# Performance work log

Hardware: AMD Instinct MI355X
Metric: run time of the kernel (lower is better)

The kernel has to match this reference:

```python
import math
import jax, jax.numpy as jnp
import numpy as np

LN_EPS = 1e-5


def _layernorm(x, g, b):
    m = jnp.mean(x, axis=-1, keepdims=True)
    v = jnp.var(x, axis=-1, keepdims=True)
    return (x - m) / jnp.sqrt(v + LN_EPS) * g + b


def setup_inputs() -> dict:
    key = jax.random.key(0)
    ks = jax.random.split(key, 14)
    B, C, H, W = 8, 96, 224, 224
    dim, hidden = 96, int(96 * 4.0)

    def lin(k, i, o):
        return jax.random.normal(k, (i, o), jnp.float32) * 0.02

    return {
        "x": jax.random.normal(ks[0], (B, C, H, W), jnp.float32),
        "entropy_map": jax.random.uniform(ks[1], (B, 1, H, W), jnp.float32),
        "beta": jnp.float32(1.0),
        "wq": lin(ks[2], dim, dim), "bq": jnp.zeros((dim,), jnp.float32),
        "wk": lin(ks[3], dim, dim), "bk": jnp.zeros((dim,), jnp.float32),
        "wv": lin(ks[4], dim, dim), "bv": jnp.zeros((dim,), jnp.float32),
        "wo": lin(ks[5], dim, dim), "bo": jnp.zeros((dim,), jnp.float32),
        "ln1_g": jnp.ones((dim,), jnp.float32), "ln1_b": jnp.zeros((dim,), jnp.float32),
        "ln2_g": jnp.ones((dim,), jnp.float32), "ln2_b": jnp.zeros((dim,), jnp.float32),
        "w_fc1": lin(ks[6], dim, hidden), "b_fc1": jnp.zeros((hidden,), jnp.float32),
        "w_fc2": lin(ks[7], hidden, dim), "b_fc2": jnp.zeros((dim,), jnp.float32),
    }


def reference(x, entropy_map, beta, wq, bq, wk, bk, wv, bv, wo, bo,
              ln1_g, ln1_b, ln2_g, ln2_b, w_fc1, b_fc1, w_fc2, b_fc2):
    B, C, H, W = x.shape
    ws = 7
    num_heads = 4
    hd = C // num_heads
    nHw, nWw = H // ws, W // ws
    N = ws * ws

    # (B,C,H,W) -> (B,H,W,C), norm1
    xt = jnp.transpose(x, (0, 2, 3, 1))
    xn = _layernorm(xt, ln1_g, ln1_b)

    # window partition -> (B*nW, N, C)
    xw = xn.reshape(B, nHw, ws, nWw, ws, C).transpose(0, 1, 3, 2, 4, 5).reshape(-1, N, C)
    ew = entropy_map.transpose(0, 2, 3, 1).reshape(B, nHw, ws, nWw, ws, 1)
    ew = ew.transpose(0, 1, 3, 2, 4, 5).reshape(-1, N, 1)  # (Bw, N, 1)

    Bw = xw.shape[0]
    q = (jnp.einsum('bnc,cd->bnd', xw, wq) + bq).reshape(Bw, N, num_heads, hd).transpose(0, 2, 1, 3)
    k = (jnp.einsum('bnc,cd->bnd', xw, wk) + bk).reshape(Bw, N, num_heads, hd).transpose(0, 2, 1, 3)
    v = (jnp.einsum('bnc,cd->bnd', xw, wv) + bv).reshape(Bw, N, num_heads, hd).transpose(0, 2, 1, 3)

    scores = jnp.einsum('bhqd,bhkd->bhqk', q, k) / math.sqrt(hd)
    attn = jax.nn.softmax(scores, axis=-1)

    # entropy gating: per-query factor (Bw,1,N,1), then renormalize over keys
    gating = jnp.exp(-beta * ew)[:, None, :, :]
    attn = attn * gating
    attn = attn / (jnp.sum(attn, axis=-1, keepdims=True) + 1e-9)

    out = jnp.einsum('bhqk,bhkd->bhqd', attn, v).transpose(0, 2, 1, 3).reshape(Bw, N, C)
    out = jnp.einsum('bnc,cd->bnd', out, wo) + bo

    # window merge -> (B,H,W,C)
    out = out.reshape(B, nHw, nWw, ws, ws, C).transpose(0, 1, 3, 2, 4, 5).reshape(B, H, W, C)

    x_res = xt + out  # (B,H,W,C)

    # MLP branch
    xn2 = _layernorm(x_res, ln2_g, ln2_b)
    h = jax.nn.gelu(jnp.einsum('bhwc,cd->bhwd', xn2, w_fc1) + b_fc1, approximate=False)
    mlp_out = jnp.einsum('bhwd,dc->bhwc', h, w_fc2) + b_fc2

    x_out = x_res + mlp_out
    return jnp.transpose(x_out, (0, 3, 1, 2))  # (B,C,H,W)
```

## Files before the change

kernel.cpp:

```cpp
#include <hip/hip_runtime.h>
#include <hip/hip_bf16.h>
#include <math.h>

typedef __attribute__((ext_vector_type(8))) short short8;
typedef __attribute__((ext_vector_type(4))) float f32x4;
typedef __attribute__((ext_vector_type(4))) unsigned int uint4v;

struct __align__(8) U2 { unsigned int x, y; };

#define DEVI static __device__ __forceinline__

DEVI unsigned pk1(float f){ unsigned u = __float_as_uint(f); return (u + 0x7fffu + ((u>>16)&1u)) >> 16; }
DEVI unsigned pk2(float a, float b){
  __hip_bfloat162 h = __float22bfloat162_rn(float2{a, b});
  union { __hip_bfloat162 h; unsigned u; } c; c.h = h; return c.u;
}
DEVI float bfu(unsigned hs){ return __uint_as_float((hs & 0xffffu) << 16); }

DEVI short8 lds8(const unsigned short* p){
  union { short8 v; U2 u[2]; } f;
  f.u[0] = *(const U2*)p;
  f.u[1] = *(const U2*)(p + 4);
  return f.v;
}
DEVI short8 mk8(unsigned a, unsigned b, unsigned c, unsigned d){
  union { short8 v; unsigned u[4]; } f; f.u[0]=a; f.u[1]=b; f.u[2]=c; f.u[3]=d; return f.v;
}
DEVI short8 zero8(){ return mk8(0,0,0,0); }
DEVI short8 gfrag(const unsigned short* p){ union { short8 v; uint4v u; } f; f.u = *(const uint4v*)p; return f.v; }
DEVI f32x4 MFMA(short8 a, short8 b, f32x4 c){ return __builtin_amdgcn_mfma_f32_16x16x32_bf16(a, b, c, 0, 0, 0); }
DEVI void st2(unsigned short* p, unsigned lo, unsigned hi){ U2 t; t.x=lo; t.y=hi; *(U2*)p = t; }

DEVI float fastrcp(float x){ float r; asm("v_rcp_f32 %0, %1" : "=v"(r) : "v"(x)); return r; }
DEVI float gelu_f(float v){
  float z2 = fmaf(v*v*v, -0.07135481627f, -1.5957691216f*v);
  return v * fastrcp(1.f + __expf(z2));
}

__global__ __launch_bounds__(256) void prep_kernel(
    const float* __restrict__ wq, const float* __restrict__ wk,
    const float* __restrict__ wv, const float* __restrict__ wo,
    const float* __restrict__ w1, const float* __restrict__ w2,
    unsigned short* __restrict__ wfr)
{
  int i = blockIdx.x * 256 + threadIdx.x;
  if (i >= 110592) return;
  int j = i & 7, lane = (i >> 3) & 63, fr = i >> 9;
  int ln = lane & 15, lg = lane >> 4;
  float v;
  if (fr < 18)      { int s = fr;       int mt = s/3,  kb = s%3;  v = wq[(32*kb + 8*lg + j)*96  + 16*mt + ln] * 0.20412414523193150818f; }
  else if (fr < 36) { int s = fr - 18;  int mt = s/3,  kb = s%3;  v = wk[(32*kb + 8*lg + j)*96  + 16*mt + ln]; }
  else if (fr < 54) { int s = fr - 36;  int mt = s/3,  kb = s%3;  v = wv[(32*kb + 8*lg + j)*96  + 16*mt + ln]; }
  else if (fr < 72) { int s = fr - 54;  int mt = s/3,  kb = s%3;  v = wo[(32*kb + 8*lg + j)*96  + 16*mt + ln]; }
  else if (fr < 144){ int s = fr - 72;  int mt = s/3,  kb = s%3;  v = w1[(32*kb + 8*lg + j)*384 + 16*mt + ln]; }
  else              { int s = fr - 144; int mt = s/12, kb = s%12; v = w2[(32*kb + 8*lg + j)*96  + 16*mt + ln]; }
  wfr[i] = (unsigned short)pk1(v);
}

__global__ __launch_bounds__(256, 3) void attn_kernel(
    const float* __restrict__ x, const float* __restrict__ emap,
    const float* __restrict__ beta_p,
    const float* __restrict__ bq, const float* __restrict__ bk,
    const float* __restrict__ bv, const float* __restrict__ bo,
    const float* __restrict__ g1, const float* __restrict__ b1,
    const unsigned short* __restrict__ wfr,
    unsigned short* __restrict__ xres)
{
  __shared__ __align__(16) char smem[48448];
  unsigned short* XN = (unsigned short*)(smem);
  unsigned short* VT = (unsigned short*)(smem);
  unsigned short* QS = (unsigned short*)(smem + 14144);
  unsigned short* KS = (unsigned short*)(smem + 26944);
  unsigned short* PB = (unsigned short*)(smem + 39744);

  const int tid = threadIdx.x;
  const int lane = tid & 63;
  const int w = tid >> 6, lg = lane >> 4, ln = lane & 15;

  int bid = blockIdx.x;
  int bw  = ((bid & 7) << 10) | (bid >> 3);
  const int b  = bw >> 10;
  const int rr = bw & 1023;
  const int h0w = (rr >> 5) * 7;
  const int w0w = (rr & 31) * 7;

  const int t = 16*w + ln;

  float xv[24];
  float ewv = 0.f;
  {
    if (t < 49){
      size_t pixloc = (size_t)(h0w + t/7)*224 + w0w + t%7;
      const float* xp = x + (size_t)(b*96 + 4*lg)*50176 + pixloc;
#pragma unroll
      for (int mt = 0; mt < 6; ++mt)
#pragma unroll
        for (int r = 0; r < 4; ++r) xv[mt*4+r] = xp[(size_t)(16*mt + r)*50176];
      ewv = emap[(size_t)b*50176 + pixloc];
    } else {
#pragma unroll
      for (int i = 0; i < 24; ++i) xv[i] = 0.f;
    }
    float s = 0.f, s2 = 0.f;
#pragma unroll
    for (int i = 0; i < 24; ++i){ s += xv[i]; s2 += xv[i]*xv[i]; }
    s  += __shfl_xor(s, 16);  s  += __shfl_xor(s, 32);
    s2 += __shfl_xor(s2, 16); s2 += __shfl_xor(s2, 32);
    float m = s * (1.f/96.f);
    float var = s2 * (1.f/96.f) - m*m;
    float rstd = rsqrtf(var + 1e-5f);
    unsigned short* row = XN + t*100;
    if (t < 49){
#pragma unroll
      for (int mt = 0; mt < 6; ++mt){
        int c0 = 16*mt + 4*lg;
        st2(row + c0,
            pk2((xv[4*mt+0]-m)*rstd*g1[c0+0]+b1[c0+0], (xv[4*mt+1]-m)*rstd*g1[c0+1]+b1[c0+1]),
            pk2((xv[4*mt+2]-m)*rstd*g1[c0+2]+b1[c0+2], (xv[4*mt+3]-m)*rstd*g1[c0+3]+b1[c0+3]));
      }
    } else {
#pragma unroll
      for (int mt = 0; mt < 6; ++mt) st2(row + 16*mt + 4*lg, 0u, 0u);
    }
  }

  short8 bx0 = lds8(XN + t*100 + 0  + 8*lg);
  short8 bx1 = lds8(XN + t*100 + 32 + 8*lg);
  short8 bx2 = lds8(XN + t*100 + 64 + 8*lg);
  __syncthreads();

  {
#pragma unroll
    for (int mt = 0; mt < 6; ++mt){
      int d0 = 16*mt + 4*lg;
      f32x4 aq, ak;
#pragma unroll
      for (int r = 0; r < 4; ++r){ aq[r] = bq[d0+r]*0.20412414523193150818f; ak[r] = bk[d0+r]; }
      aq = MFMA(gfrag(wfr +        (mt*3+0)*512 + lane*8), bx0, aq);
      aq = MFMA(gfrag(wfr +        (mt*3+1)*512 + lane*8), bx1, aq);
      aq = MFMA(gfrag(wfr +        (mt*3+2)*512 + lane*8), bx2, aq);
      ak = MFMA(gfrag(wfr + 9216 + (mt*3+0)*512 + lane*8), bx0, ak);
      ak = MFMA(gfrag(wfr + 9216 + (mt*3+1)*512 + lane*8), bx1, ak);
      ak = MFMA(gfrag(wfr + 9216 + (mt*3+2)*512 + lane*8), bx2, ak);
      st2(QS + t*100 + d0, pk2(aq[0],aq[1]), pk2(aq[2],aq[3]));
      st2(KS + t*100 + d0, pk2(ak[0],ak[1]), pk2(ak[2],ak[3]));
    }
#pragma unroll
    for (int mt = 0; mt < 6; ++mt){
      int d0 = 16*mt + 4*lg;
      f32x4 av;
#pragma unroll
      for (int r = 0; r < 4; ++r) av[r] = bv[d0+r];
      av = MFMA(gfrag(wfr + 18432 + (mt*3+0)*512 + lane*8), bx0, av);
      av = MFMA(gfrag(wfr + 18432 + (mt*3+1)*512 + lane*8), bx1, av);
      av = MFMA(gfrag(wfr + 18432 + (mt*3+2)*512 + lane*8), bx2, av);
#pragma unroll
      for (int r = 0; r < 4; ++r) VT[(d0+r)*68 + t] = (unsigned short)pk1(av[r]);
    }
  }
  __syncthreads();

  const float beta = beta_p[0];
  const float gq   = __expf(-beta * ewv);
  const float gfac = gq / (gq + 1e-9f);

  f32x4 mz;  mz[0]=0.f; mz[1]=0.f; mz[2]=0.f; mz[3]=0.f;
  f32x4 m3;
#pragma unroll
  for (int r = 0; r < 4; ++r) m3[r] = (4*lg + r >= 1) ? -50.f : 0.f;

  unsigned short* PBw = PB + (w*16 + ln)*68;

#pragma unroll
  for (int hp = 0; hp < 2; ++hp){
    const int h0 = 2*hp, h1 = 2*hp + 1;

    short8 bqf0 = (lg < 3) ? lds8(QS + t*100 + 24*h0 + 8*lg) : zero8();
    short8 bqf1 = (lg < 3) ? lds8(QS + t*100 + 24*h1 + 8*lg) : zero8();
    f32x4 sv0[4], sv1[4];
#pragma unroll
    for (int mt = 0; mt < 4; ++mt){
      short8 af0 = (lg < 3) ? lds8(KS + (16*mt+ln)*100 + 24*h0 + 8*lg) : zero8();
      short8 af1 = (lg < 3) ? lds8(KS + (16*mt+ln)*100 + 24*h1 + 8*lg) : zero8();
      f32x4 ci = (mt == 3) ? m3 : mz;
      sv0[mt] = MFMA(af0, bqf0, ci);
      sv1[mt] = MFMA(af1, bqf1, ci);
    }

    float vv0[16], vv1[16];
    float ss0 = 0.f, ss1 = 0.f;
#pragma unroll
    for (int i = 0; i < 16; ++i){
      float e0 = __expf(sv0[i>>2][i&3]); vv0[i] = e0; ss0 += e0;
      float e1 = __expf(sv1[i>>2][i&3]); vv1[i] = e1; ss1 += e1;
    }
    ss0 += __shfl_xor(ss0, 16);  ss1 += __shfl_xor(ss1, 16);
    ss0 += __shfl_xor(ss0, 32);  ss1 += __shfl_xor(ss1, 32);
    float inv0 = gfac * fastrcp(ss0);
    float inv1 = gfac * fastrcp(ss1);

#pragma unroll
    for (int mt = 0; mt < 4; ++mt)
      st2(PBw + 16*mt + 4*lg,
          pk2(vv0[4*mt+0], vv0[4*mt+1]), pk2(vv0[4*mt+2], vv0[4*mt+3]));
    short8 pf00 = lds8(PBw + 0  + 8*lg);
    short8 pf01 = lds8(PBw + 32 + 8*lg);

#pragma unroll
    for (int mt = 0; mt < 4; ++mt)
      st2(PBw + 16*mt + 4*lg,
          pk2(vv1[4*mt+0], vv1[4*mt+1]), pk2(vv1[4*mt+2], vv1[4*mt+3]));
    short8 pf10 = lds8(PBw + 0  + 8*lg);
    short8 pf11 = lds8(PBw + 32 + 8*lg);

#pragma unroll
    for (int mt = 0; mt < 2; ++mt){
      f32x4 pv0; pv0[0]=0.f; pv0[1]=0.f; pv0[2]=0.f; pv0[3]=0.f;
      f32x4 pv1; pv1[0]=0.f; pv1[1]=0.f; pv1[2]=0.f; pv1[3]=0.f;
      pv0 = MFMA(lds8(VT + (24*h0+16*mt+ln)*68 + 0  + 8*lg), pf00, pv0);
      pv1 = MFMA(lds8(VT + (24*h1+16*mt+ln)*68 + 0  + 8*lg), pf10, pv1);
      pv0 = MFMA(lds8(VT + (24*h0+16*mt+ln)*68 + 32 + 8*lg), pf01, pv0);
      pv1 = MFMA(lds8(VT + (24*h1+16*mt+ln)*68 + 32 + 8*lg), pf11, pv1);
      if (!(mt == 1 && lg >= 2)){
        st2(QS + t*100 + 24*h0 + 16*mt + 4*lg,
            pk2(pv0[0]*inv0, pv0[1]*inv0), pk2(pv0[2]*inv0, pv0[3]*inv0));
        st2(QS + t*100 + 24*h1 + 16*mt + 4*lg,
            pk2(pv1[0]*inv1, pv1[1]*inv1), pk2(pv1[2]*inv1, pv1[3]*inv1));
      }
    }
  }

  {
    f32x4 po[6];
#pragma unroll
    for (int mt = 0; mt < 6; ++mt){
      int c0 = 16*mt + 4*lg;
#pragma unroll
      for (int r = 0; r < 4; ++r) po[mt][r] = bo[c0+r];
    }
#pragma unroll
    for (int kb = 0; kb < 3; ++kb){
      short8 bf_ = lds8(QS + t*100 + 32*kb + 8*lg);
#pragma unroll
      for (int mt = 0; mt < 6; ++mt)
        po[mt] = MFMA(gfrag(wfr + 27648 + (mt*3+kb)*512 + lane*8), bf_, po[mt]);
    }
    if (t < 49){
      size_t pixloc = (size_t)(h0w + t/7)*224 + w0w + t%7;
      unsigned short* xo = xres + ((size_t)b*50176 + pixloc)*96;
#pragma unroll
      for (int mt = 0; mt < 6; ++mt){
        int c0 = 16*mt + 4*lg;
        st2(xo + c0,
            pk2(po[mt][0] + xv[4*mt+0], po[mt][1] + xv[4*mt+1]),
            pk2(po[mt][2] + xv[4*mt+2], po[mt][3] + xv[4*mt+3]));
      }
    }
  }
}

__global__ __launch_bounds__(256, 3) void mlp_kernel(
    const unsigned short* __restrict__ xres,
    const float* __restrict__ g2, const float* __restrict__ b2,
    const float* __restrict__ bf1, const float* __restrict__ bf2,
    const unsigned short* __restrict__ wfr,
    float* __restrict__ out)
{
  __shared__ __align__(16) unsigned short XH[4][6400];
  const int tid = threadIdx.x, lane = tid & 63, w = tid >> 6;
  const int lg = lane >> 4, ln = lane & 15;
  unsigned short* XN2 = &XH[w][0];
  unsigned short* HS  = &XH[w][3200];

  const int tile = blockIdx.x*4 + w;
  const size_t p0 = (size_t)tile * 32;
  const int bimg = (int)(p0 / 50176);
  const size_t pixin = p0 - (size_t)bimg*50176;

#pragma unroll
  for (int s = 0; s < 2; ++s){
    const unsigned* xp = (const unsigned*)(xres + (p0 + 16*s + (size_t)ln)*96 + 24*lg);
    float xv[24];
#pragma unroll
    for (int i = 0; i < 12; ++i){
      unsigned u = xp[i];
      xv[2*i] = bfu(u); xv[2*i+1] = bfu(u >> 16);
    }
    float sm = 0.f, s2 = 0.f;
#pragma unroll
    for (int i = 0; i < 24; ++i){ sm += xv[i]; s2 += xv[i]*xv[i]; }
    sm += __shfl_xor(sm, 16);  sm += __shfl_xor(sm, 32);
    s2 += __shfl_xor(s2, 16);  s2 += __shfl_xor(s2, 32);
    float m = sm * (1.f/96.f);
    float var = s2 * (1.f/96.f) - m*m;
    float rstd = rsqrtf(var + 1e-5f);
    unsigned* w32 = (unsigned*)(XN2 + (16*s + ln)*100 + 24*lg);
#pragma unroll
    for (int i = 0; i < 12; ++i){
      int c = 24*lg + 2*i;
      w32[i] = pk2((xv[2*i]   - m)*rstd*g2[c]   + b2[c],
                   (xv[2*i+1] - m)*rstd*g2[c+1] + b2[c+1]);
    }
  }

  f32x4 oaccA[6], oaccB[6];
#pragma unroll
  for (int mt = 0; mt < 6; ++mt){
    int c0 = 16*mt + 4*lg;
#pragma unroll
    for (int r = 0; r < 4; ++r){ oaccA[mt][r] = bf2[c0+r]; oaccB[mt][r] = bf2[c0+r]; }
  }

  short8 bxA0 = lds8(XN2 + ln*100 + 0  + 8*lg);
  short8 bxA1 = lds8(XN2 + ln*100 + 32 + 8*lg);
  short8 bxA2 = lds8(XN2 + ln*100 + 64 + 8*lg);
  short8 bxB0 = lds8(XN2 + (16+ln)*100 + 0  + 8*lg);
  short8 bxB1 = lds8(XN2 + (16+ln)*100 + 32 + 8*lg);
  short8 bxB2 = lds8(XN2 + (16+ln)*100 + 64 + 8*lg);

#pragma unroll
  for (int p = 0; p < 4; ++p){
#pragma unroll
    for (int mt = 0; mt < 6; ++mt){
      int hg = p*96 + 16*mt + 4*lg;
      f32x4 hA, hB;
#pragma unroll
      for (int r = 0; r < 4; ++r){ hA[r] = bf1[hg+r]; hB[r] = bf1[hg+r]; }
      short8 a0 = gfrag(wfr + 36864 + ((p*6+mt)*3+0)*512 + lane*8);
      short8 a1 = gfrag(wfr + 36864 + ((p*6+mt)*3+1)*512 + lane*8);
      short8 a2 = gfrag(wfr + 36864 + ((p*6+mt)*3+2)*512 + lane*8);
      hA = MFMA(a0, bxA0, hA); hB = MFMA(a0, bxB0, hB);
      hA = MFMA(a1, bxA1, hA); hB = MFMA(a1, bxB1, hB);
      hA = MFMA(a2, bxA2, hA); hB = MFMA(a2, bxB2, hB);
      st2(HS + ln*100 + 16*mt + 4*lg,
          pk2(gelu_f(hA[0]), gelu_f(hA[1])), pk2(gelu_f(hA[2]), gelu_f(hA[3])));
      st2(HS + (16+ln)*100 + 16*mt + 4*lg,
          pk2(gelu_f(hB[0]), gelu_f(hB[1])), pk2(gelu_f(hB[2]), gelu_f(hB[3])));
    }
#pragma unroll
    for (int kb = 0; kb < 3; ++kb){
      short8 bhA = lds8(HS + ln*100      + 32*kb + 8*lg);
      short8 bhB = lds8(HS + (16+ln)*100 + 32*kb + 8*lg);
#pragma unroll
      for (int mt = 0; mt < 6; ++mt){
        short8 af = gfrag(wfr + 73728 + (mt*12 + p*3 + kb)*512 + lane*8);
        oaccA[mt] = MFMA(af, bhA, oaccA[mt]);
        oaccB[mt] = MFMA(af, bhB, oaccB[mt]);
      }
    }
  }

  {
    const unsigned short* xrA = xres + (p0 + (size_t)ln)*96;
    const unsigned short* xrB = xrA + 16*96;
    float* obA = out + (size_t)bimg*96*50176 + pixin + ln;
    float* obB = obA + 16;
#pragma unroll
    for (int mt = 0; mt < 6; ++mt){
      int c0 = 16*mt + 4*lg;
      U2 rA = *(const U2*)(xrA + c0);
      U2 rB = *(const U2*)(xrB + c0);
      obA[(size_t)(c0+0)*50176] = oaccA[mt][0] + bfu(rA.x);
      obA[(size_t)(c0+1)*50176] = oaccA[mt][1] + bfu(rA.x >> 16);
      obA[(size_t)(c0+2)*50176] = oaccA[mt][2] + bfu(rA.y);
      obA[(size_t)(c0+3)*50176] = oaccA[mt][3] + bfu(rA.y >> 16);
      obB[(size_t)(c0+0)*50176] = oaccB[mt][0] + bfu(rB.x);
      obB[(size_t)(c0+1)*50176] = oaccB[mt][1] + bfu(rB.x >> 16);
      obB[(size_t)(c0+2)*50176] = oaccB[mt][2] + bfu(rB.y);
      obB[(size_t)(c0+3)*50176] = oaccB[mt][3] + bfu(rB.y >> 16);
    }
  }
}

extern "C" void kernel_launch(void* const* d_in, const int* in_sizes, int n_in,
                              void* d_out, int out_size, void* d_ws, size_t ws_size,
                              hipStream_t stream) {
  const float* x    = (const float*)d_in[0];
  const float* emap = (const float*)d_in[1];
  const float* beta = (const float*)d_in[2];
  const float* wq   = (const float*)d_in[3];
  const float* bq   = (const float*)d_in[4];
  const float* wk   = (const float*)d_in[5];
  const float* bk   = (const float*)d_in[6];
  const float* wv   = (const float*)d_in[7];
  const float* bv   = (const float*)d_in[8];
  const float* wo   = (const float*)d_in[9];
  const float* bo   = (const float*)d_in[10];
  const float* g1   = (const float*)d_in[11];
  const float* b1   = (const float*)d_in[12];
  const float* g2   = (const float*)d_in[13];
  const float* b2   = (const float*)d_in[14];
  const float* w1   = (const float*)d_in[15];
  const float* bf1  = (const float*)d_in[16];
  const float* w2   = (const float*)d_in[17];
  const float* bf2  = (const float*)d_in[18];

  float* out = (float*)d_out;
  unsigned short* wfr  = (unsigned short*)d_ws;
  unsigned short* xres = (unsigned short*)((char*)d_ws + 262144);

  prep_kernel<<<dim3(432), dim3(256), 0, stream>>>(wq, wk, wv, wo, w1, w2, wfr);
  attn_kernel<<<dim3(8192), dim3(256), 0, stream>>>(
      x, emap, beta, bq, bk, bv, bo, g1, b1, wfr, xres);
  mlp_kernel<<<dim3(3136), dim3(256), 0, stream>>>(
      xres, g2, b2, bf1, bf2, wfr, out);
}
```

Before: 353.7 us.

## Split attention into dense-token QKV projection kernel and per-window attention kernel

The fused per-window attention kernel is split in two. The first kernel computes LayerNorm and the Q/K/V projections over densely packed tokens: 32 tokens per wave, no padding, with weight fragments reused across two token tiles. It writes bf16 Q/K/V and the gating factor to global memory. The second kernel reads them per window to do softmax attention and the output projection. This removes the padding waste of 49-token windows in 64-row tiles and lightens LDS use, at the cost of an extra global round-trip for Q/K/V and x being read twice.

Result: slower. 606.2 us (+71.4%).

```diff
diff --git a/kernel.cpp b/kernel.cpp
--- a/kernel.cpp
+++ b/kernel.cpp
@@ -57,6 +57,233 @@
   wfr[i] = (unsigned short)pk1(v);
 }
 
+__global__ __launch_bounds__(256, 4) void qkv_a(
+    const float* __restrict__ x, const float* __restrict__ emap,
+    const float* __restrict__ beta_p,
+    const float* __restrict__ bq, const float* __restrict__ bk,
+    const float* __restrict__ bv,
+    const float* __restrict__ g1, const float* __restrict__ b1,
+    const unsigned short* __restrict__ wfr,
+    unsigned short* __restrict__ QB, unsigned short* __restrict__ KB,
+    unsigned short* __restrict__ VB, float* __restrict__ GQ)
+{
+  const int tid = threadIdx.x, lane = tid & 63, w = tid >> 6;
+  const int lg = lane >> 4, ln = lane & 15;
+  const int base = (blockIdx.x*4 + w) * 32;
+  const float beta = beta_p[0];
+
+  short8 bx[2][3];
+#pragma unroll
+  for (int u = 0; u < 2; ++u){
+    int wtok = base + 16*u + ln;
+    int win = wtok / 49, ii = wtok - win*49;
+    int pr = ii / 7, pc = ii - pr*7;
+    int bimg = win >> 10, rr = win & 1023;
+    size_t pixloc = (size_t)((rr >> 5)*7 + pr)*224 + (rr & 31)*7 + pc;
+    const float* xp = x + (size_t)(bimg*96 + 8*lg)*50176 + pixloc;
+    float xv[24];
+#pragma unroll
+    for (int kb = 0; kb < 3; ++kb)
+#pragma unroll
+      for (int j = 0; j < 8; ++j)
+        xv[kb*8+j] = xp[(size_t)(32*kb + j)*50176];
+    float s = 0.f, s2 = 0.f;
+#pragma unroll
+    for (int i = 0; i < 24; ++i){ s += xv[i]; s2 += xv[i]*xv[i]; }
+    s  += __shfl_xor(s, 16);  s  += __shfl_xor(s, 32);
+    s2 += __shfl_xor(s2, 16); s2 += __shfl_xor(s2, 32);
+    float m = s * (1.f/96.f);
+    float var = s2 * (1.f/96.f) - m*m;
+    float rstd = rsqrtf(var + 1e-5f);
+#pragma unroll
+    for (int kb = 0; kb < 3; ++kb){
+      int c = 32*kb + 8*lg;
+      unsigned u0 = pk2((xv[kb*8+0]-m)*rstd*g1[c+0]+b1[c+0], (xv[kb*8+1]-m)*rstd*g1[c+1]+b1[c+1]);
+      unsigned u1 = pk2((xv[kb*8+2]-m)*rstd*g1[c+2]+b1[c+2], (xv[kb*8+3]-m)*rstd*g1[c+3]+b1[c+3]);
+      unsigned u2 = pk2((xv[kb*8+4]-m)*rstd*g1[c+4]+b1[c+4], (xv[kb*8+5]-m)*rstd*g1[c+5]+b1[c+5]);
+      unsigned u3 = pk2((xv[kb*8+6]-m)*rstd*g1[c+6]+b1[c+6], (xv[kb*8+7]-m)*rstd*g1[c+7]+b1[c+7]);
+      bx[u][kb] = mk8(u0, u1, u2, u3);
+    }
+    if (lg == 0)
+      GQ[wtok] = __expf(-beta * emap[(size_t)bimg*50176 + pixloc]);
+  }
+
+#pragma unroll
+  for (int mtx = 0; mtx < 3; ++mtx){
+    const unsigned short* wbase_ = wfr + mtx*9216;
+    const float* bias = (mtx == 0) ? bq : (mtx == 1) ? bk : bv;
+    unsigned short* OUT = (mtx == 0) ? QB : (mtx == 1) ? KB : VB;
+    const float bsc = (mtx == 0) ? 0.20412414523193150818f : 1.0f;
+#pragma unroll
+    for (int mt = 0; mt < 6; ++mt){
+      int d0 = 16*mt + 4*lg;
+      short8 a0 = gfrag(wbase_ + (mt*3+0)*512 + lane*8);
+      short8 a1 = gfrag(wbase_ + (mt*3+1)*512 + lane*8);
+      short8 a2 = gfrag(wbase_ + (mt*3+2)*512 + lane*8);
+#pragma unroll
+      for (int u = 0; u < 2; ++u){
+        f32x4 acc;
+#pragma unroll
+        for (int r = 0; r < 4; ++r) acc[r] = bias[d0+r] * bsc;
+        acc = MFMA(a0, bx[u][0], acc);
+        acc = MFMA(a1, bx[u][1], acc);
+        acc = MFMA(a2, bx[u][2], acc);
+        st2(OUT + (size_t)(base + 16*u + ln)*96 + d0,
+            pk2(acc[0],acc[1]), pk2(acc[2],acc[3]));
+      }
+    }
+  }
+}
+
+__global__ __launch_bounds__(256, 4) void attn_b(
+    const float* __restrict__ x,
+    const unsigned short* __restrict__ QB, const unsigned short* __restrict__ KB,
+    const unsigned short* __restrict__ VB, const float* __restrict__ GQ,
+    const float* __restrict__ bo,
+    const unsigned short* __restrict__ wfr,
+    unsigned short* __restrict__ xres)
+{
+  __shared__ __align__(16) char smem[35648];
+  unsigned short* VT = (unsigned short*)(smem);
+  unsigned short* OS = (unsigned short*)(smem + 14144);
+  unsigned short* PB = (unsigned short*)(smem + 26944);
+
+  const int tid = threadIdx.x, lane = tid & 63;
+  const int w = tid >> 6, lg = lane >> 4, ln = lane & 15;
+
+  int bid = blockIdx.x;
+  int bw  = ((bid & 7) << 10) | (bid >> 3);
+  const int b  = bw >> 10;
+  const int rr = bw & 1023;
+  const int h0w = (rr >> 5) * 7;
+  const int w0w = (rr & 31) * 7;
+  const size_t wbase = (size_t)bw * 49;
+  const int t = 16*w + ln;
+  const bool tv = (t < 49);
+
+  float xv[24];
+  size_t pixloc = 0;
+  if (tv){
+    pixloc = (size_t)(h0w + t/7)*224 + w0w + t%7;
+    const float* xp = x + (size_t)(b*96 + 4*lg)*50176 + pixloc;
+#pragma unroll
+    for (int mt = 0; mt < 6; ++mt)
+#pragma unroll
+      for (int r = 0; r < 4; ++r) xv[mt*4+r] = xp[(size_t)(16*mt + r)*50176];
+  } else {
+#pragma unroll
+    for (int i = 0; i < 24; ++i) xv[i] = 0.f;
+  }
+  float gqv = GQ[wbase + t];
+
+  {
+    const unsigned short* vrow = VB + (wbase + t)*96;
+#pragma unroll
+    for (int mt = 0; mt < 6; ++mt){
+      int d0 = 16*mt + 4*lg;
+      U2 u = *(const U2*)(vrow + d0);
+      VT[(d0+0)*68 + t] = (unsigned short)(u.x & 0xffffu);
+      VT[(d0+1)*68 + t] = (unsigned short)(u.x >> 16);
+      VT[(d0+2)*68 + t] = (unsigned short)(u.y & 0xffffu);
+      VT[(d0+3)*68 + t] = (unsigned short)(u.y >> 16);
+    }
+  }
+  __syncthreads();
+
+  const float gfac = gqv / (gqv + 1e-9f);
+  f32x4 mz;  mz[0]=0.f; mz[1]=0.f; mz[2]=0.f; mz[3]=0.f;
+  f32x4 m3;
+#pragma unroll
+  for (int r = 0; r < 4; ++r) m3[r] = (4*lg + r >= 1) ? -50.f : 0.f;
+
+  unsigned short* PBw = PB + (w*16 + ln)*68;
+
+#pragma unroll
+  for (int hp = 0; hp < 2; ++hp){
+    const int h0 = 2*hp, h1 = 2*hp + 1;
+
+    short8 bqf0 = (lg < 3) ? gfrag(QB + (wbase + t)*96 + 24*h0 + 8*lg) : zero8();
+    short8 bqf1 = (lg < 3) ? gfrag(QB + (wbase + t)*96 + 24*h1 + 8*lg) : zero8();
+    f32x4 sv0[4], sv1[4];
+#pragma unroll
+    for (int mt = 0; mt < 4; ++mt){
+      short8 af0 = (lg < 3) ? gfrag(KB + (wbase + 16*mt + ln)*96 + 24*h0 + 8*lg) : zero8();
+      short8 af1 = (lg < 3) ? gfrag(KB + (wbase + 16*mt + ln)*96 + 24*h1 + 8*lg) : zero8();
+      f32x4 ci = (mt == 3) ? m3 : mz;
+      sv0[mt] = MFMA(af0, bqf0, ci);
+      sv1[mt] = MFMA(af1, bqf1, ci);
+    }
+
+    float vv0[16], vv1[16];
+    float ss0 = 0.f, ss1 = 0.f;
+#pragma unroll
+    for (int i = 0; i < 16; ++i){
+      float e0 = __expf(sv0[i>>2][i&3]); vv0[i] = e0; ss0 += e0;
+      float e1 = __expf(sv1[i>>2][i&3]); vv1[i] = e1; ss1 += e1;
+    }
+    ss0 += __shfl_xor(ss0, 16);  ss1 += __shfl_xor(ss1, 16);
+    ss0 += __shfl_xor(ss0, 32);  ss1 += __shfl_xor(ss1, 32);
+    float inv0 = gfac * fastrcp(ss0);
+    float inv1 = gfac * fastrcp(ss1);
+
+#pragma unroll
+    for (int mt = 0; mt < 4; ++mt)
+      st2(PBw + 16*mt + 4*lg,
+          pk2(vv0[4*mt+0], vv0[4*mt+1]), pk2(vv0[4*mt+2], vv0[4*mt+3]));
+    short8 pf00 = lds8(PBw + 0  + 8*lg);
+    short8 pf01 = lds8(PBw + 32 + 8*lg);
+#pragma unroll
+    for (int mt = 0; mt < 4; ++mt)
+      st2(PBw + 16*mt + 4*lg,
+          pk2(vv1[4*mt+0], vv1[4*mt+1]), pk2(vv1[4*mt+2], vv1[4*mt+3]));
+    short8 pf10 = lds8(PBw + 0  + 8*lg);
+    short8 pf11 = lds8(PBw + 32 + 8*lg);
+
+#pragma unroll
+    for (int mt = 0; mt < 2; ++mt){
+      f32x4 pv0; pv0[0]=0.f; pv0[1]=0.f; pv0[2]=0.f; pv0[3]=0.f;
+      f32x4 pv1; pv1[0]=0.f; pv1[1]=0.f; pv1[2]=0.f; pv1[3]=0.f;
+      pv0 = MFMA(lds8(VT + (24*h0+16*mt+ln)*68 + 0  + 8*lg), pf00, pv0);
+      pv1 = MFMA(lds8(VT + (24*h1+16*mt+ln)*68 + 0  + 8*lg), pf10, pv1);
+      pv0 = MFMA(lds8(VT + (24*h0+16*mt+ln)*68 + 32 + 8*lg), pf01, pv0);
+      pv1 = MFMA(lds8(VT + (24*h1+16*mt+ln)*68 + 32 + 8*lg), pf11, pv1);
+      if (!(mt == 1 && lg >= 2)){
+        st2(OS + t*100 + 24*h0 + 16*mt + 4*lg,
+            pk2(pv0[0]*inv0, pv0[1]*inv0), pk2(pv0[2]*inv0, pv0[3]*inv0));
+        st2(OS + t*100 + 24*h1 + 16*mt + 4*lg,
+            pk2(pv1[0]*inv1, pv1[1]*inv1), pk2(pv1[2]*inv1, pv1[3]*inv1));
+      }
+    }
+  }
+
+  {
+    f32x4 po[6];
+#pragma unroll
+    for (int mt = 0; mt < 6; ++mt){
+      int c0 = 16*mt + 4*lg;
+#pragma unroll
+      for (int r = 0; r < 4; ++r) po[mt][r] = bo[c0+r];
+    }
+#pragma unroll
+    for (int kb = 0; kb < 3; ++kb){
+      short8 bf_ = lds8(OS + t*100 + 32*kb + 8*lg);
+#pragma unroll
+      for (int mt = 0; mt < 6; ++mt)
+        po[mt] = MFMA(gfrag(wfr + 27648 + (mt*3+kb)*512 + lane*8), bf_, po[mt]);
+    }
+    if (tv){
+      unsigned short* xo = xres + ((size_t)b*50176 + pixloc)*96;
+#pragma unroll
+      for (int mt = 0; mt < 6; ++mt){
+        int c0 = 16*mt + 4*lg;
+        st2(xo + c0,
+            pk2(po[mt][0] + xv[4*mt+0], po[mt][1] + xv[4*mt+1]),
+            pk2(po[mt][2] + xv[4*mt+2], po[mt][3] + xv[4*mt+3]));
+      }
+    }
+  }
+}
+
 __global__ __launch_bounds__(256, 3) void attn_kernel(
     const float* __restrict__ x, const float* __restrict__ emap,
     const float* __restrict__ beta_p,
@@ -73,8 +300,7 @@
   unsigned short* KS = (unsigned short*)(smem + 26944);
   unsigned short* PB = (unsigned short*)(smem + 39744);
 
-  const int tid = threadIdx.x;
-  const int lane = tid & 63;
+  const int tid = threadIdx.x, lane = tid & 63;
   const int w = tid >> 6, lg = lane >> 4, ln = lane & 15;
 
   int bid = blockIdx.x;
@@ -83,11 +309,9 @@
   const int rr = bw & 1023;
   const int h0w = (rr >> 5) * 7;
   const int w0w = (rr & 31) * 7;
-
   const int t = 16*w + ln;
 
-  float xv[24];
-  float ewv = 0.f;
+  float xv[24]; float ewv = 0.f;
   {
     if (t < 49){
       size_t pixloc = (size_t)(h0w + t/7)*224 + w0w + t%7;
@@ -123,12 +347,10 @@
       for (int mt = 0; mt < 6; ++mt) st2(row + 16*mt + 4*lg, 0u, 0u);
     }
   }
-
   short8 bx0 = lds8(XN + t*100 + 0  + 8*lg);
   short8 bx1 = lds8(XN + t*100 + 32 + 8*lg);
   short8 bx2 = lds8(XN + t*100 + 64 + 8*lg);
   __syncthreads();
-
   {
 #pragma unroll
     for (int mt = 0; mt < 6; ++mt){
@@ -163,18 +385,15 @@
   const float beta = beta_p[0];
   const float gq   = __expf(-beta * ewv);
   const float gfac = gq / (gq + 1e-9f);
-
   f32x4 mz;  mz[0]=0.f; mz[1]=0.f; mz[2]=0.f; mz[3]=0.f;
   f32x4 m3;
 #pragma unroll
   for (int r = 0; r < 4; ++r) m3[r] = (4*lg + r >= 1) ? -50.f : 0.f;
-
   unsigned short* PBw = PB + (w*16 + ln)*68;
 
 #pragma unroll
   for (int hp = 0; hp < 2; ++hp){
     const int h0 = 2*hp, h1 = 2*hp + 1;
-
     short8 bqf0 = (lg < 3) ? lds8(QS + t*100 + 24*h0 + 8*lg) : zero8();
     short8 bqf1 = (lg < 3) ? lds8(QS + t*100 + 24*h1 + 8*lg) : zero8();
     f32x4 sv0[4], sv1[4];
@@ -186,7 +405,6 @@
       sv0[mt] = MFMA(af0, bqf0, ci);
       sv1[mt] = MFMA(af1, bqf1, ci);
     }
-
     float vv0[16], vv1[16];
     float ss0 = 0.f, ss1 = 0.f;
 #pragma unroll
@@ -198,21 +416,18 @@
     ss0 += __shfl_xor(ss0, 32);  ss1 += __shfl_xor(ss1, 32);
     float inv0 = gfac * fastrcp(ss0);
     float inv1 = gfac * fastrcp(ss1);
-
 #pragma unroll
     for (int mt = 0; mt < 4; ++mt)
       st2(PBw + 16*mt + 4*lg,
           pk2(vv0[4*mt+0], vv0[4*mt+1]), pk2(vv0[4*mt+2], vv0[4*mt+3]));
     short8 pf00 = lds8(PBw + 0  + 8*lg);
     short8 pf01 = lds8(PBw + 32 + 8*lg);
-
 #pragma unroll
     for (int mt = 0; mt < 4; ++mt)
       st2(PBw + 16*mt + 4*lg,
           pk2(vv1[4*mt+0], vv1[4*mt+1]), pk2(vv1[4*mt+2], vv1[4*mt+3]));
     short8 pf10 = lds8(PBw + 0  + 8*lg);
     short8 pf11 = lds8(PBw + 32 + 8*lg);
-
 #pragma unroll
     for (int mt = 0; mt < 2; ++mt){
       f32x4 pv0; pv0[0]=0.f; pv0[1]=0.f; pv0[2]=0.f; pv0[3]=0.f;
@@ -229,7 +444,6 @@
       }
     }
   }
-
   {
     f32x4 po[6];
 #pragma unroll
@@ -396,12 +610,42 @@
   const float* bf2  = (const float*)d_in[18];
 
   float* out = (float*)d_out;
-  unsigned short* wfr  = (unsigned short*)d_ws;
-  unsigned short* xres = (unsigned short*)((char*)d_ws + 262144);
+  unsigned short* wfr = (unsigned short*)d_ws;
+
+  const size_t ROWB = 401472ull * 96 * 2;
+  const size_t QOFF  = 262144;
+  const size_t KOFF  = QOFF + ROWB;
+  const size_t VOFF  = KOFF + ROWB;
+  const size_t GQOFF = VOFF + ROWB;
+  const size_t XROFF = GQOFF + 401472ull*4;
+  const size_t NEED  = XROFF + 401408ull*96*2;
 
   prep_kernel<<<dim3(432), dim3(256), 0, stream>>>(wq, wk, wv, wo, w1, w2, wfr);
-  attn_kernel<<<dim3(8192), dim3(256), 0, stream>>>(
-      x, emap, beta, bq, bk, bv, bo, g1, b1, wfr, xres);
-  mlp_kernel<<<dim3(3136), dim3(256), 0, stream>>>(
-      xres, g2, b2, bf1, bf2, wfr, out);
-}
+
+  if (ws_size >= NEED) {
+    unsigned short* QB = (unsigned short*)((char*)d_ws + QOFF);
+    unsigned short* KB = (unsigned short*)((char*)d_ws + KOFF);
+    unsigned short* VB = (unsigned short*)((char*)d_ws + VOFF);
+    float* GQ          = (float*)((char*)d_ws + GQOFF);
+    unsigned short* xres = (unsigned short*)((char*)d_ws + XROFF);
+
+    const size_t PADOFF = 401408ull * 192;
+    hipMemsetAsync((char*)QB + PADOFF, 0, 64*192, stream);
+    hipMemsetAsync((char*)KB + PADOFF, 0, 64*192, stream);
+    hipMemsetAsync((char*)VB + PADOFF, 0, 64*192, stream);
+    hipMemsetAsync((char*)GQ + 401408ull*4, 0, 64*4, stream);
+
+    qkv_a<<<dim3(3136), dim3(256), 0, stream>>>(
+        x, emap, beta, bq, bk, bv, g1, b1, wfr, QB, KB, VB, GQ);
+    attn_b<<<dim3(8192), dim3(256), 0, stream>>>(
+        x, QB, KB, VB, GQ, bo, wfr, xres);
+    mlp_kernel<<<dim3(3136), dim3(256), 0, stream>>>(
+        xres, g2, b2, bf1, bf2, wfr, out);
+  } else {
+    unsigned short* xres = (unsigned short*)((char*)d_ws + 262144);
+    attn_kernel<<<dim3(8192), dim3(256), 0, stream>>>(
+        x, emap, beta, bq, bk, bv, bo, g1, b1, wfr, xres);
+    mlp_kernel<<<dim3(3136), dim3(256), 0, stream>>>(
+        xres, g2, b2, bf1, bf2, wfr, out);
+  }
+}
```
